# Performance work log

Hardware: AMD Instinct MI355X
Metric: run time of the kernel (lower is better)

The kernel has to match this reference:

```python
import jax, jax.numpy as jnp
import numpy as np

MARGIN = 0.0625  # init kwarg `margin`; barrier = relu


def setup_inputs() -> dict:
    key = jax.random.key(0)
    k1, k2, k3, k4 = jax.random.split(key, 4)
    B, N, M = 64, 64, 100000
    return {
        "outputs": jax.random.normal(k1, (B, N, 3), dtype=jnp.float32),
        "c2ws": jax.random.normal(k2, (B, 4, 4), dtype=jnp.float32),
        "scene_scales": jax.random.uniform(k3, (B,), dtype=jnp.float32),
        "means": jax.random.normal(k4, (M, 3), dtype=jnp.float32),
    }


def reference(outputs, c2ws, scene_scales, means):
    # aff = R * s (per-batch scaled rotation block), trans = translation column
    aff = c2ws[:, :3, :3] * scene_scales[:, None, None]      # [B,3,3]
    trans = c2ws[:, :3, 3]                                   # [B,3]
    # retrajs = baddbmm(trans, outputs, aff.mT) = outputs @ aff^T + trans
    retrajs = jnp.einsum("bnj,bij->bni", outputs, aff) + trans[:, None, :]
    q = retrajs.reshape(-1, 3)                               # [Q,3], Q = B*N
    # Brute-force nearest neighbor (replaces kd_tree.query); torch_kdtree
    # returns SQUARED euclidean distances, so we keep d^2.
    # d2[q,m] = |q|^2 + |m|^2 - 2 q.m  -> [Q,M] (the dominant memory-bound op)
    d2 = (
        jnp.sum(q * q, axis=-1, keepdims=True)
        + jnp.sum(means * means, axis=-1)[None, :]
        - 2.0 * (q @ means.T)
    )
    dists = jnp.maximum(jnp.min(d2, axis=1), 0.0)            # [Q]
    loss = jnp.mean(jax.nn.relu(-(dists - MARGIN)))
    return loss
```

## Files before the change

### kernel.cpp

```cpp
#include <hip/hip_runtime.h>
#include <hip/hip_bf16.h>

#define MARGIN 0.0625f

#define B 64
#define N 64
#define P 4096
#define M 100000
#define G 512
#define QS 2
#define CHUNK 196
#define MPAD 100352
#define R 8
#define H 16
#define GPERH 32

#define WS_MPACK_OFF   0
#define WS_QBUF_OFF    1605632
#define WS_PARTIAL_OFF 1671168
#define WS_PART2_OFF   0

__global__ __launch_bounds__(256) void prep_kernel(
    const float* __restrict__ outputs,
    const float* __restrict__ c2ws,
    const float* __restrict__ scales,
    const float* __restrict__ means,
    float4* __restrict__ mpack,
    float4* __restrict__ qbuf,
    float* __restrict__ out)
{
    int idx = blockIdx.x * 256 + threadIdx.x;
    if (idx == 0) out[0] = 0.0f;
    if (idx < MPAD) {
        if (idx < M) {
            float x = means[3 * idx + 0];
            float y = means[3 * idx + 1];
            float z = means[3 * idx + 2];
            float mm = fmaf(x, x, fmaf(y, y, z * z));
            mpack[idx] = make_float4(-2.0f * x, -2.0f * y, -2.0f * z, mm);
        } else {
            mpack[idx] = make_float4(0.0f, 0.0f, 0.0f, 1e30f);
        }
    }
    if (idx < P) {
        int b = idx >> 6;
        float s  = scales[b];
        float o0 = outputs[3 * idx + 0];
        float o1 = outputs[3 * idx + 1];
        float o2 = outputs[3 * idx + 2];
        const float* cw = c2ws + b * 16;
        float q0 = fmaf(s, fmaf(cw[0],  o0, fmaf(cw[1],  o1, cw[2]  * o2)), cw[3]);
        float q1 = fmaf(s, fmaf(cw[4],  o0, fmaf(cw[5],  o1, cw[6]  * o2)), cw[7]);
        float q2 = fmaf(s, fmaf(cw[8],  o0, fmaf(cw[9],  o1, cw[10] * o2)), cw[11]);
        float qq = fmaf(q0, q0, fmaf(q1, q1, q2 * q2));
        qbuf[idx] = make_float4(q0, q1, q2, qq);
    }
}

__global__ __launch_bounds__(256) void nn_kernel(
    const float4* __restrict__ mpack,
    const float4* __restrict__ qbuf,
    float* __restrict__ partial)
{
    const int t  = threadIdx.x;
    const int g  = blockIdx.x;
    const int qs = blockIdx.y;
    const int base  = g * CHUNK;
    const int pbase = qs * (P / QS);

    float qx[R], qy[R], qz[R], mn[R];
#pragma unroll
    for (int i = 0; i < R; ++i) {
        float4 q = qbuf[pbase + i * 256 + t];
        qx[i] = q.x; qy[i] = q.y; qz[i] = q.z;
        mn[i] = 1e30f;
    }

#pragma unroll 2
    for (int k = 0; k < CHUNK; k += 2) {
        float4 m0 = mpack[base + k];
        float4 m1 = mpack[base + k + 1];
#pragma unroll
        for (int i = 0; i < R; ++i) {
            float d0 = fmaf(qx[i], m0.x, fmaf(qy[i], m0.y, fmaf(qz[i], m0.z, m0.w)));
            float d1 = fmaf(qx[i], m1.x, fmaf(qy[i], m1.y, fmaf(qz[i], m1.z, m1.w)));
            mn[i] = fminf(fminf(d0, d1), mn[i]);
        }
    }

#pragma unroll
    for (int i = 0; i < R; ++i) {
        int p = pbase + i * 256 + t;
        float qq = qbuf[p].w;
        partial[g * P + p] = fmaxf(qq + mn[i], 0.0f);
    }
}

__global__ __launch_bounds__(256) void reduce1_kernel(
    const float* __restrict__ partial,
    float* __restrict__ partial2)
{
    const int t = threadIdx.x;
    const int s = blockIdx.x;
    const int h = blockIdx.y;
    const int p = s * 256 + t;

    float m = 1e30f;
#pragma unroll
    for (int j = 0; j < GPERH; ++j)
        m = fminf(m, partial[(h * GPERH + j) * P + p]);

    partial2[h * P + p] = m;
}

__global__ __launch_bounds__(256) void reduce2_kernel(
    const float* __restrict__ partial2,
    float* __restrict__ out)
{
    const int t = threadIdx.x;
    const int p = blockIdx.x * 256 + t;

    float m = 1e30f;
#pragma unroll
    for (int h = 0; h < H; ++h)
        m = fminf(m, partial2[h * P + p]);

    float v = fmaxf(MARGIN - m, 0.0f) * (1.0f / (float)P);

#pragma unroll
    for (int off = 32; off > 0; off >>= 1)
        v += __shfl_down(v, off, 64);

    __shared__ float lds[4];
    int wid = t >> 6;
    if ((t & 63) == 0) lds[wid] = v;
    __syncthreads();
    if (t == 0)
        atomicAdd(out, lds[0] + lds[1] + lds[2] + lds[3]);
}

extern "C" void kernel_launch(void* const* d_in, const int* in_sizes, int n_in,
                              void* d_out, int out_size, void* d_ws, size_t ws_size,
                              hipStream_t stream) {
    const float* outputs = (const float*)d_in[0];
    const float* c2ws    = (const float*)d_in[1];
    const float* scales  = (const float*)d_in[2];
    const float* means   = (const float*)d_in[3];

    char* ws = (char*)d_ws;
    float4* mpack   = (float4*)(ws + WS_MPACK_OFF);
    float4* qbuf    = (float4*)(ws + WS_QBUF_OFF);
    float* partial  = (float*)(ws + WS_PARTIAL_OFF);
    float* partial2 = (float*)(ws + WS_PART2_OFF);
    float* out      = (float*)d_out;

    prep_kernel<<<(MPAD + 255) / 256, 256, 0, stream>>>(outputs, c2ws, scales,
                                                        means, mpack, qbuf, out);
    nn_kernel<<<dim3(G, QS), 256, 0, stream>>>(mpack, qbuf, partial);
    reduce1_kernel<<<dim3(16, H), 256, 0, stream>>>(partial, partial2);
    reduce2_kernel<<<16, 256, 0, stream>>>(partial2, out);
}
```

Before: 110.8 us.

## Fuse prep into NN kernel, use packed FP32 math, merge reductions

Removes the separate prep kernel. Each NN block now computes its query transform itself and reads raw means directly, computing |m|^2 on the fly with register double-buffering. The distance loop uses 2-wide float vectors so the compiler can emit packed FMA/min instructions. The chunking changes to 500x200, so no padding is needed. The two reduction kernels merge into one that reduces across four waves through LDS. This saves two launches and the mpack and qbuf round-trips, in exchange for redundant query-transform and norm work in every block.

```diff
diff --git a/kernel.cpp b/kernel.cpp
--- a/kernel.cpp
+++ b/kernel.cpp
@@ -7,136 +7,126 @@
 #define N 64
 #define P 4096
 #define M 100000
-#define G 512
+#define G 500
+#define CHUNK 200
 #define QS 2
-#define CHUNK 196
-#define MPAD 100352
 #define R 8
-#define H 16
-#define GPERH 32
+#define NB 4
+#define GRP 8
+#define NIT (CHUNK / GRP)
+#define SEG 4
+#define GPERSEG (G / SEG)
 
-#define WS_MPACK_OFF   0
-#define WS_QBUF_OFF    1605632
-#define WS_PARTIAL_OFF 1671168
-#define WS_PART2_OFF   0
+typedef float float2v __attribute__((ext_vector_type(2)));
 
-__global__ __launch_bounds__(256) void prep_kernel(
+
+__global__ __launch_bounds__(256) void nn_kernel(
     const float* __restrict__ outputs,
     const float* __restrict__ c2ws,
     const float* __restrict__ scales,
     const float* __restrict__ means,
-    float4* __restrict__ mpack,
-    float4* __restrict__ qbuf,
+    float* __restrict__ partial,
     float* __restrict__ out)
 {
-    int idx = blockIdx.x * 256 + threadIdx.x;
-    if (idx == 0) out[0] = 0.0f;
-    if (idx < MPAD) {
-        if (idx < M) {
-            float x = means[3 * idx + 0];
-            float y = means[3 * idx + 1];
-            float z = means[3 * idx + 2];
-            float mm = fmaf(x, x, fmaf(y, y, z * z));
-            mpack[idx] = make_float4(-2.0f * x, -2.0f * y, -2.0f * z, mm);
-        } else {
-            mpack[idx] = make_float4(0.0f, 0.0f, 0.0f, 1e30f);
-        }
-    }
-    if (idx < P) {
-        int b = idx >> 6;
+    const int t  = threadIdx.x;
+    const int g  = blockIdx.x;
+    const int qs = blockIdx.y;
+    if (g == 0 && qs == 0 && t == 0) out[0] = 0.0f;
+
+    const int pbase = qs * (P / QS);
+
+    float2v qxn[NB], qyn[NB], qzn[NB], mn[NB];
+    float qq[R];
+#pragma unroll
+    for (int i = 0; i < R; ++i) {
+        int p = pbase + i * 256 + t;
+        int b = p >> 6;
         float s  = scales[b];
-        float o0 = outputs[3 * idx + 0];
-        float o1 = outputs[3 * idx + 1];
-        float o2 = outputs[3 * idx + 2];
+        float o0 = outputs[3 * p + 0];
+        float o1 = outputs[3 * p + 1];
+        float o2 = outputs[3 * p + 2];
         const float* cw = c2ws + b * 16;
         float q0 = fmaf(s, fmaf(cw[0],  o0, fmaf(cw[1],  o1, cw[2]  * o2)), cw[3]);
         float q1 = fmaf(s, fmaf(cw[4],  o0, fmaf(cw[5],  o1, cw[6]  * o2)), cw[7]);
         float q2 = fmaf(s, fmaf(cw[8],  o0, fmaf(cw[9],  o1, cw[10] * o2)), cw[11]);
-        float qq = fmaf(q0, q0, fmaf(q1, q1, q2 * q2));
-        qbuf[idx] = make_float4(q0, q1, q2, qq);
-    }
-}
-
-__global__ __launch_bounds__(256) void nn_kernel(
-    const float4* __restrict__ mpack,
-    const float4* __restrict__ qbuf,
-    float* __restrict__ partial)
-{
-    const int t  = threadIdx.x;
-    const int g  = blockIdx.x;
-    const int qs = blockIdx.y;
-    const int base  = g * CHUNK;
-    const int pbase = qs * (P / QS);
-
-    float qx[R], qy[R], qz[R], mn[R];
-#pragma unroll
-    for (int i = 0; i < R; ++i) {
-        float4 q = qbuf[pbase + i * 256 + t];
-        qx[i] = q.x; qy[i] = q.y; qz[i] = q.z;
-        mn[i] = 1e30f;
+        qq[i] = fmaf(q0, q0, fmaf(q1, q1, q2 * q2));
+        qxn[i >> 1][i & 1] = -2.0f * q0;
+        qyn[i >> 1][i & 1] = -2.0f * q1;
+        qzn[i >> 1][i & 1] = -2.0f * q2;
+        mn [i >> 1][i & 1] = 1e30f;
     }
 
-#pragma unroll 2
-    for (int k = 0; k < CHUNK; k += 2) {
-        float4 m0 = mpack[base + k];
-        float4 m1 = mpack[base + k + 1];
+    const float* mp = means + 3 * g * CHUNK;
+    float cur[3 * GRP], nxt[3 * GRP];
 #pragma unroll
-        for (int i = 0; i < R; ++i) {
-            float d0 = fmaf(qx[i], m0.x, fmaf(qy[i], m0.y, fmaf(qz[i], m0.z, m0.w)));
-            float d1 = fmaf(qx[i], m1.x, fmaf(qy[i], m1.y, fmaf(qz[i], m1.z, m1.w)));
-            mn[i] = fminf(fminf(d0, d1), mn[i]);
+    for (int c = 0; c < 3 * GRP; ++c) cur[c] = mp[c];
+
+    for (int it = 0; it < NIT; ++it) {
+        const float* nx = mp + 3 * GRP * (it + 1);
+        if (it < NIT - 1) {
+#pragma unroll
+            for (int c = 0; c < 3 * GRP; ++c) nxt[c] = nx[c];
+        }
+#pragma unroll
+        for (int j = 0; j < GRP; j += 2) {
+            float x0 = cur[3 * j + 0], y0 = cur[3 * j + 1], z0 = cur[3 * j + 2];
+            float x1 = cur[3 * j + 3], y1 = cur[3 * j + 4], z1 = cur[3 * j + 5];
+            float mm0 = fmaf(x0, x0, fmaf(y0, y0, z0 * z0));
+            float mm1 = fmaf(x1, x1, fmaf(y1, y1, z1 * z1));
+            float2v vx0 = {x0, x0}, vy0 = {y0, y0}, vz0 = {z0, z0}, vm0 = {mm0, mm0};
+            float2v vx1 = {x1, x1}, vy1 = {y1, y1}, vz1 = {z1, z1}, vm1 = {mm1, mm1};
+#pragma unroll
+            for (int u = 0; u < NB; ++u) {
+                float2v d0 = __builtin_elementwise_fma(qxn[u], vx0,
+                             __builtin_elementwise_fma(qyn[u], vy0,
+                             __builtin_elementwise_fma(qzn[u], vz0, vm0)));
+                float2v d1 = __builtin_elementwise_fma(qxn[u], vx1,
+                             __builtin_elementwise_fma(qyn[u], vy1,
+                             __builtin_elementwise_fma(qzn[u], vz1, vm1)));
+                mn[u] = __builtin_elementwise_min(mn[u],
+                        __builtin_elementwise_min(d0, d1));
+            }
+        }
+        if (it < NIT - 1) {
+#pragma unroll
+            for (int c = 0; c < 3 * GRP; ++c) cur[c] = nxt[c];
         }
     }
 
 #pragma unroll
     for (int i = 0; i < R; ++i) {
         int p = pbase + i * 256 + t;
-        float qq = qbuf[p].w;
-        partial[g * P + p] = fmaxf(qq + mn[i], 0.0f);
+        partial[g * P + p] = fmaxf(qq[i] + mn[i >> 1][i & 1], 0.0f);
     }
 }
 
-__global__ __launch_bounds__(256) void reduce1_kernel(
+__global__ __launch_bounds__(256) void reduce_kernel(
     const float* __restrict__ partial,
-    float* __restrict__ partial2)
-{
-    const int t = threadIdx.x;
-    const int s = blockIdx.x;
-    const int h = blockIdx.y;
-    const int p = s * 256 + t;
-
-    float m = 1e30f;
-#pragma unroll
-    for (int j = 0; j < GPERH; ++j)
-        m = fminf(m, partial[(h * GPERH + j) * P + p]);
-
-    partial2[h * P + p] = m;
-}
-
-__global__ __launch_bounds__(256) void reduce2_kernel(
-    const float* __restrict__ partial2,
     float* __restrict__ out)
 {
     const int t = threadIdx.x;
-    const int p = blockIdx.x * 256 + t;
+    const int w = t >> 6;
+    const int l = t & 63;
+    const int p = blockIdx.x * 64 + l;
 
     float m = 1e30f;
+#pragma unroll 5
+    for (int gi = 0; gi < GPERSEG; ++gi)
+        m = fminf(m, partial[(w * GPERSEG + gi) * P + p]);
+
+    __shared__ float lds[SEG][64];
+    lds[w][l] = m;
+    __syncthreads();
+
+    if (t < 64) {
+        m = fminf(fminf(lds[0][l], lds[1][l]), fminf(lds[2][l], lds[3][l]));
+        float v = fmaxf(MARGIN - m, 0.0f) * (1.0f / (float)P);
 #pragma unroll
-    for (int h = 0; h < H; ++h)
-        m = fminf(m, partial2[h * P + p]);
-
-    float v = fmaxf(MARGIN - m, 0.0f) * (1.0f / (float)P);
-
-#pragma unroll
-    for (int off = 32; off > 0; off >>= 1)
-        v += __shfl_down(v, off, 64);
-
-    __shared__ float lds[4];
-    int wid = t >> 6;
-    if ((t & 63) == 0) lds[wid] = v;
-    __syncthreads();
-    if (t == 0)
-        atomicAdd(out, lds[0] + lds[1] + lds[2] + lds[3]);
+        for (int off = 32; off > 0; off >>= 1)
+            v += __shfl_down(v, off, 64);
+        if (l == 0)
+            atomicAdd(out, v);
+    }
 }
 
 extern "C" void kernel_launch(void* const* d_in, const int* in_sizes, int n_in,
@@ -147,16 +137,10 @@
     const float* scales  = (const float*)d_in[2];
     const float* means   = (const float*)d_in[3];
 
-    char* ws = (char*)d_ws;
-    float4* mpack   = (float4*)(ws + WS_MPACK_OFF);
-    float4* qbuf    = (float4*)(ws + WS_QBUF_OFF);
-    float* partial  = (float*)(ws + WS_PARTIAL_OFF);
-    float* partial2 = (float*)(ws + WS_PART2_OFF);
-    float* out      = (float*)d_out;
+    float* partial = (float*)d_ws;
+    float* out     = (float*)d_out;
 
-    prep_kernel<<<(MPAD + 255) / 256, 256, 0, stream>>>(outputs, c2ws, scales,
-                                                        means, mpack, qbuf, out);
-    nn_kernel<<<dim3(G, QS), 256, 0, stream>>>(mpack, qbuf, partial);
-    reduce1_kernel<<<dim3(16, H), 256, 0, stream>>>(partial, partial2);
-    reduce2_kernel<<<16, 256, 0, stream>>>(partial2, out);
+    nn_kernel<<<dim3(G, QS), 256, 0, stream>>>(outputs, c2ws, scales, means,
+                                               partial, out);
+    reduce_kernel<<<64, 256, 0, stream>>>(partial, out);
 }
```

Result: slower. 121.6 us (+9.7%).
